# Optimization experiments

Hardware: AMD Instinct MI355X
Metric: run time of the kernel (lower is better)

## Reference

```python
import jax, jax.numpy as jnp
import numpy as np

B, T, HID, MC, L, NCLS = 256, 128, 64, 30, 2, 100


def _flow(x, t, fW0, fb0, fW1, fb1, fW2, fb2, ftw):
    # Continuous affine coupling flow (stribor). x: [..., S, HID], t: [..., S, 1]
    hid = x.shape[-1]
    base = (jnp.arange(hid) < hid // 2).astype(x.dtype)  # ordered_0 mask
    for l in range(fW0.shape[0]):
        m = base if l % 2 == 0 else 1.0 - base
        z = x * m
        a = jnp.tanh(jnp.concatenate([z, t], -1) @ fW0[l] + fb0[l])
        a = jnp.tanh(a @ fW1[l] + fb1[l])
        ss = a @ fW2[l] + fb2[l]                      # [..., 2*hid]
        scale, shift = jnp.split(ss, 2, -1)
        t_scale, t_shift = jnp.split(jnp.tanh(t * ftw[l]), 2, -1)  # TimeTanh
        x = z + (1.0 - m) * (x * jnp.exp(scale * t_scale) + shift * t_shift)
    return x


def setup_inputs() -> dict:
    key = jax.random.key(0)
    ks = jax.random.split(key, 12)
    n = lambda k, s, sc=0.1: jax.random.normal(k, s, dtype=jnp.float32) * sc
    return {
        "times": jax.random.uniform(ks[0], (B, T, 1), dtype=jnp.float32),
        "marks": jax.random.randint(ks[1], (B, T, 1), 0, NCLS),
        "mask": jnp.ones((B, T, 1), jnp.float32),
        "u": jax.random.uniform(ks[2], (T, MC, 1), dtype=jnp.float32),
        "emb": n(ks[3], (NCLS, HID), 1.0),
        "fW0": n(ks[4], (L, HID + 1, HID)),
        "fb0": jnp.zeros((L, HID), jnp.float32),
        "fW1": n(ks[5], (L, HID, HID)),
        "fb1": jnp.zeros((L, HID), jnp.float32),
        "fW2": n(ks[6], (L, HID, 2 * HID)),
        "fb2": jnp.zeros((L, 2 * HID), jnp.float32),
        "ftw": n(ks[7], (L, 2 * HID), 1.0),
        "Wi": n(ks[8], (HID, 1)),
        "bi": jnp.zeros((1,), jnp.float32),
        "W_ih": n(ks[9], (4 * HID, 1 + HID)),
        "W_hh": n(ks[10], (4 * HID, HID)),
        "b_ih": jnp.zeros((4 * HID,), jnp.float32),
        "b_hh": jnp.zeros((4 * HID,), jnp.float32),
    }


def reference(times, marks, mask, u, emb, fW0, fb0, fW1, fb1, fW2, fb2, ftw,
              Wi, bi, W_ih, W_hh, b_ih, b_hh):
    Bn, Tn, _ = times.shape
    hid = emb.shape[1]
    mc = u.shape[1]
    marks_e = emb[marks[..., 0]]      # [B,T,hid]
    m1 = marks_e[:, 1]                # source uses marks[:, 1] every step (faithful)
    inten = lambda x: jax.nn.softplus(x @ Wi + bi)

    def step(carry, xs):
        h, c = carry                  # h,c: [B,hid]
        t, u_i = xs                   # t: [B,1], u_i: [mc,1]
        t3 = t[:, None, :]            # [B,1,1]
        ts = u_i[None] * t3           # [B,mc,1] MC time samples in [0,t)
        xb = jnp.broadcast_to(h[:, None, :], (Bn, mc, hid))
        path = _flow(xb, ts, fW0, fb0, fW1, fb1, fW2, fb2, ftw)   # [B,mc,hid]
        integral = inten(path).mean(1, keepdims=True) * t3        # [B,1,1]
        h2 = _flow(h[:, None, :], t3, fW0, fb0, fW1, fb1, fW2, fb2, ftw)  # [B,1,hid]
        lam = inten(h2)                                           # [B,1,1]
        gates = jnp.concatenate([t, m1], -1) @ W_ih.T + b_ih + h2[:, 0] @ W_hh.T + b_hh
        ig, fg, gg, og = jnp.split(gates, 4, -1)
        c_n = jax.nn.sigmoid(fg) * c + jax.nn.sigmoid(ig) * jnp.tanh(gg)
        h_n = jax.nn.sigmoid(og) * jnp.tanh(c_n)
        nll = -jnp.log(lam[:, 0]) + integral[:, 0]                # [B,1]
        return (h_n, c_n), (h2[:, 0], nll)

    h0 = jnp.zeros((Bn, hid), times.dtype)
    (_, _), (hidden, nll) = jax.lax.scan(step, (h0, h0), (jnp.swapaxes(times, 0, 1), u))
    hidden = jnp.swapaxes(hidden, 0, 1)                           # [B,T,hid]
    loss = (jnp.swapaxes(nll, 0, 1)[:, :, :] * mask[..., 0][..., None]).sum() / mask.sum()
    return loss, hidden
```

## Files before the change

### kernel.cpp

```cpp
#include <hip/hip_runtime.h>
#include <hip/hip_bf16.h>
#include <math.h>

#define Bn   256
#define Tn   128
#define HID  64
#define MCn  30

typedef __attribute__((ext_vector_type(8))) short bf16x8;
typedef __attribute__((ext_vector_type(4))) float f32x4;

__device__ __forceinline__ float rcp_(float x) { return __builtin_amdgcn_rcpf(x); }
__device__ __forceinline__ float tanhf_(float x) {
    float e = __expf(-2.0f * x);
    return __builtin_fmaf(2.0f, rcp_(1.0f + e), -1.0f);
}
__device__ __forceinline__ float sigmoidf_(float x) {
    return rcp_(1.0f + __expf(-x));
}
__device__ __forceinline__ float softplusf_(float z) {
    float e = __expf(-fabsf(z));
    return fmaxf(z, 0.0f) + __logf(1.0f + e);
}
__device__ __forceinline__ unsigned short f2b(float f) {
    union { float f; unsigned u; } v; v.f = f;
    unsigned r = v.u + 0x7FFF + ((v.u >> 16) & 1);
    return (unsigned short)(r >> 16);
}
__device__ __forceinline__ unsigned pk2(float a, float b) {
    union { __hip_bfloat162 h2; unsigned u; } cv;
    cv.h2 = __float22bfloat162_rn(make_float2(a, b));
    return cv.u;
}

extern "C" __global__ __launch_bounds__(256)
void prep_kernel(const int* __restrict__ marks, const float* __restrict__ mask,
                 const float* __restrict__ emb, const float* __restrict__ fW0,
                 const float* __restrict__ fW1, const float* __restrict__ fW2,
                 const float* __restrict__ fb0, const float* __restrict__ fb1,
                 const float* __restrict__ fb2, const float* __restrict__ ftw,
                 const float* __restrict__ Wi, const float* __restrict__ W_ih,
                 const float* __restrict__ W_hh,
                 const float* __restrict__ b_ih, const float* __restrict__ b_hh,
                 float* __restrict__ gc, float* __restrict__ invd,
                 float* __restrict__ parv, unsigned short* __restrict__ parwb,
                 float* __restrict__ seqw1T, float* __restrict__ seqw2T,
                 float* __restrict__ whh260)
{
    __shared__ float red[4];
    const int blk = blockIdx.x, tid = threadIdx.x;
    if (blk < Bn) {
        const int mark = marks[blk * Tn + 1];
        const float* er = emb + mark * HID;
        const float* wr = W_ih + tid * 65 + 1;
        float acc = b_ih[tid] + b_hh[tid];
        #pragma unroll
        for (int k = 0; k < HID; k++) acc += er[k] * wr[k];
        gc[blk * 256 + tid] = acc;
    } else if (blk == Bn) {
        float s = 0.f;
        for (int i = tid; i < Bn * Tn; i += 256) s += mask[i];
        #pragma unroll
        for (int off = 32; off >= 1; off >>= 1) s += __shfl_xor(s, off, 64);
        if ((tid & 63) == 0) red[tid >> 6] = s;
        __syncthreads();
        if (tid == 0) invd[0] = 1.0f / (red[0] + red[1] + red[2] + red[3]);
    } else if (blk == Bn + 1) {
        if (tid < 128) {
            int l = tid >> 6, m = tid & 63;
            parv[tid]       = fb0[tid];
            parv[128 + tid] = fW0[(l * 65 + 64) * 64 + m];
            parv[256 + tid] = fb1[tid];
            int act = 32 * (1 - l);
            parv[384 + tid] = fb2[l * 128 + act + (m & 31) + 64 * (m >> 5)];
        }
        if (tid < 64) {
            int l = tid >> 5, i2 = tid & 31, act = 32 * (1 - l);
            parv[512 + tid] = ftw[l * 128 + act + i2];
            parv[576 + tid] = ftw[l * 128 + 64 + act + i2];
            parv[640 + tid] = Wi[tid];
            parv[704 + tid] = 0.f;
        }
    } else if (blk == Bn + 2) {
        for (int i = tid; i < 5120; i += 256) {
            int k = i % 40, m = (i / 40) & 63, l = i / 2560;
            float v = (k < 32) ? fW0[(l * 65 + 32 * l + k) * 64 + m] : 0.f;
            parwb[i] = f2b(v);
        }
    } else if (blk == Bn + 3) {
        for (int i = tid; i < 9216; i += 256) {
            int k = i % 72, m = (i / 72) & 63, l = i / 4608;
            float v = (k < 64) ? fW1[(l * 64 + k) * 64 + m] : 0.f;
            parwb[5120 + i] = f2b(v);
        }
    } else if (blk == Bn + 4) {
        for (int i = tid; i < 9216; i += 256) {
            int k = i % 72, m = (i / 72) & 63, l = i / 4608;
            int act = 32 * (1 - l);
            float v = (k < 64) ? fW2[(l * 64 + k) * 128 + act + (m & 31) + 64 * (m >> 5)] : 0.f;
            parwb[14336 + i] = f2b(v);
        }
    } else if (blk == Bn + 5) {
        for (int i = tid; i < 8704; i += 256) {
            int k = i % 68, j = (i / 68) & 63, l = i / 4352;
            seqw1T[i] = (k < 64) ? fW1[(l * 64 + k) * 64 + j] : 0.f;
        }
    } else if (blk == Bn + 6) {
        for (int i = tid; i < 8704; i += 256) {
            int k = i % 68, j = (i / 68) & 63, l = i / 4352;
            int act = 32 * (1 - l);
            seqw2T[i] = (k < 64) ?
                fW2[(l * 64 + k) * 128 + act + (j & 31) + 64 * (j >> 5)] : 0.f;
        }
    } else {
        for (int i = tid; i < 16640; i += 256) {
            int j = i / 260, rem = i % 260, k = rem >> 2, r = rem & 3;
            whh260[i] = (k < 64) ? W_hh[(r * 64 + j) * 64 + k] : 0.f;
        }
    }
}

extern "C" __global__ __launch_bounds__(192, 1)
void fused_kernel(const float* __restrict__ times, const float* __restrict__ mask,
                  const float* __restrict__ u,
                  const float* __restrict__ fW0, const float* __restrict__ fb0,
                  const float* __restrict__ fb1, const float* __restrict__ fb2,
                  const float* __restrict__ ftw, const float* __restrict__ Wi,
                  const float* __restrict__ bi, const float* __restrict__ W_ih,
                  const float* __restrict__ gc, const float* __restrict__ seqw1T,
                  const float* __restrict__ parv,
                  const unsigned short* __restrict__ parwb,
                  const float* __restrict__ invd, float* __restrict__ out)
{
    const int tid  = threadIdx.x;
    const int lane = tid & 63;
    const int w    = tid >> 6;
    const int b    = blockIdx.x;
    const int quad = lane >> 4, l15 = lane & 15;

    extern __shared__ float smem[];
    float* w1l  = smem;
    float* w2l  = smem + 8704;
    float* whhl = smem + 17408;
    float* tl   = smem + 34048;
    float* ml   = smem + 34176;
    float* xl   = smem + 34304;
    float* al   = smem + 34368;
    float* ssl  = smem + 34432;
    float* hbuf = smem + 34496;
    float* pr   = smem + 34624;
    unsigned short* csact = (unsigned short*)(smem + 34628);
    unsigned short* csxk1 = csact + 2304;
    unsigned short* csx0  = csxk1 + 1280;

    {
        const float4* s = (const float4*)seqw1T;
        float4* d = (float4*)smem;
        for (int i = tid; i < 8512; i += 192) d[i] = s[i];
        for (int i = tid; i < 128; i += 192) {
            tl[i] = times[b * Tn + i];
            ml[i] = mask[b * Tn + i];
        }
    }

    const float bi0 = bi[0];
    const float idn = invd[0];

    float w0c[2][32], w0tc[2], b0c[2], b1c[2], b2c[2], ftsc[2], ftsh[2];
    float wih0[4], gcr[4], wij = 0.f;
    float h = 0.f, c = 0.f, nllacc = 0.f;
    if (w == 0) {
        #pragma unroll
        for (int l = 0; l < 2; l++) {
            #pragma unroll
            for (int kk = 0; kk < 32; kk++)
                w0c[l][kk] = fW0[(l * 65 + 32 * l + kk) * 64 + lane];
            w0tc[l] = fW0[(l * 65 + 64) * 64 + lane];
            b0c[l]  = fb0[l * 64 + lane];
            b1c[l]  = fb1[l * 64 + lane];
            const int act = 32 * (1 - l);
            b2c[l]  = fb2[l * 128 + act + (lane & 31) + 64 * (lane >> 5)];
            ftsc[l] = ftw[l * 128 + lane];
            ftsh[l] = ftw[l * 128 + 64 + lane];
        }
        wij = Wi[lane];
        #pragma unroll
        for (int r = 0; r < 4; r++) {
            wih0[r] = W_ih[(r * 64 + lane) * 65];
            gcr[r]  = gc[b * 256 + r * 64 + lane];
        }
    }
    const int cw = w - 1;
    unsigned short* myact = csact + cw * 1152;
    unsigned short* myxk  = csxk1 + cw * 640;
    unsigned short* myx0  = csx0  + cw * 40;
    const int mc  = cw * 16 + l15;
    const bool valmc = (w > 0) && (mc < MCn);
    float wacc = 0.f;

    __syncthreads();

    for (int t = 0; t < Tn; t++) {
        if (w == 0) hbuf[(t & 1) * 64 + lane] = h;
        __syncthreads();

        if (w == 0) {
            const float tb = tl[t];
            float tscv[2], tshv[2];
            #pragma unroll
            for (int l = 0; l < 2; l++) {
                tscv[l] = tanhf_(tb * ftsc[l]);
                tshv[l] = tanhf_(tb * ftsh[l]);
            }
            float x = h;
            xl[lane] = x;
            #pragma unroll
            for (int l = 0; l < 2; l++) {
                const int kb  = 32 * l;
                const int act = 32 * (1 - l);
                {
                    float p0 = b0c[l] + tb * w0tc[l], p1 = 0.f, p2 = 0.f, p3 = 0.f;
                    const float4* xv4 = (const float4*)(xl + kb);
                    #pragma unroll
                    for (int k4 = 0; k4 < 8; k4++) {
                        float4 xv = xv4[k4];
                        p0 += xv.x * w0c[l][4 * k4 + 0];
                        p1 += xv.y * w0c[l][4 * k4 + 1];
                        p2 += xv.z * w0c[l][4 * k4 + 2];
                        p3 += xv.w * w0c[l][4 * k4 + 3];
                    }
                    al[lane] = tanhf_((p0 + p1) + (p2 + p3));
                }
                {
                    float p0 = b1c[l], p1 = 0.f, p2 = 0.f, p3 = 0.f;
                    const float4* av4 = (const float4*)al;
                    const float*  wp  = w1l + (l * 64 + lane) * 68;
                    #pragma unroll
                    for (int k4 = 0; k4 < 16; k4++) {
                        float4 av = av4[k4];
                        float4 wv = *(const float4*)(wp + 4 * k4);
                        p0 += av.x * wv.x; p1 += av.y * wv.y;
                        p2 += av.z * wv.z; p3 += av.w * wv.w;
                    }
                    al[lane] = tanhf_((p0 + p1) + (p2 + p3));
                }
                {
                    float p0 = b2c[l], p1 = 0.f, p2 = 0.f, p3 = 0.f;
                    const float4* av4 = (const float4*)al;
                    const float*  wp  = w2l + (l * 64 + lane) * 68;
                    #pragma unroll
                    for (int k4 = 0; k4 < 16; k4++) {
                        float4 av = av4[k4];
                        float4 wv = *(const float4*)(wp + 4 * k4);
                        p0 += av.x * wv.x; p1 += av.y * wv.y;
                        p2 += av.z * wv.z; p3 += av.w * wv.w;
                    }
                    ssl[lane] = (p0 + p1) + (p2 + p3);
                }
                const int idx = (lane - act) & 31;
                const float scl = ssl[idx];
                const float shf = ssl[idx + 32];
                const float xa  = x * __expf(scl * tscv[l]) + shf * tshv[l];
                const bool active = (l == 0) ? (lane >= 32) : (lane < 32);
                x = active ? xa : x;
                xl[lane] = x;
            }
            out[1 + (b * Tn + t) * 64 + lane] = x;
            float v = x * wij;
            #pragma unroll
            for (int off = 32; off >= 1; off >>= 1) v += __shfl_xor(v, off, 64);
            nllacc += -__logf(softplusf_(v + bi0)) * ml[t];
            float g0 = gcr[0] + tb * wih0[0];
            float g1 = gcr[1] + tb * wih0[1];
            float g2 = gcr[2] + tb * wih0[2];
            float g3 = gcr[3] + tb * wih0[3];
            {
                const float*  wr_base = whhl + lane * 260;
                const float4* hv4 = (const float4*)xl;
                #pragma unroll
                for (int k4 = 0; k4 < 16; k4++) {
                    float4 hv = hv4[k4];
                    const float* wr = wr_base + 16 * k4;
                    float4 wa = *(const float4*)(wr);
                    float4 wb = *(const float4*)(wr + 4);
                    float4 wc = *(const float4*)(wr + 8);
                    float4 wd = *(const float4*)(wr + 12);
                    g0 += hv.x * wa.x; g1 += hv.x * wa.y; g2 += hv.x * wa.z; g3 += hv.x * wa.w;
                    g0 += hv.y * wb.x; g1 += hv.y * wb.y; g2 += hv.y * wb.z; g3 += hv.y * wb.w;
                    g0 += hv.z * wc.x; g1 += hv.z * wc.y; g2 += hv.z * wc.z; g3 += hv.z * wc.w;
                    g0 += hv.w * wd.x; g1 += hv.w * wd.y; g2 += hv.w * wd.z; g3 += hv.w * wd.w;
                }
            }
            c = sigmoidf_(g1) * c + sigmoidf_(g0) * tanhf_(g2);
            h = sigmoidf_(g3) * tanhf_(c);
        } else {
            const float tb = tl[t];
            const float ts   = valmc ? u[t * MCn + mc] * tb : 0.f;
            const float sclf = valmc ? tb * (1.0f / 30.0f) * idn * ml[t] : 0.f;
            const float* hb  = hbuf + (t & 1) * 64;
            f32x4 xr[4];
            #pragma unroll
            for (int mt = 0; mt < 4; mt++)
                xr[mt] = *(const f32x4*)(hb + mt * 16 + quad * 4);
            if (lane < 32) myx0[lane] = f2b(hb[lane]);
            #pragma unroll
            for (int l = 0; l < 2; l++) {
                const unsigned short* wA1 = parwb + l * 2560;
                const unsigned short* wA2 = parwb + 5120 + l * 4608;
                const unsigned short* wA3 = parwb + 14336 + l * 4608;
                f32x4 c1[4];
                {
                    bf16x8 bfin = (l == 0) ? *(const bf16x8*)(myx0 + quad * 8)
                                           : *(const bf16x8*)(myxk + l15 * 40 + quad * 8);
                    #pragma unroll
                    for (int mt = 0; mt < 4; mt++) {
                        bf16x8 af = *(const bf16x8*)(wA1 + (mt * 16 + l15) * 40 + quad * 8);
                        f32x4 z = {0.f, 0.f, 0.f, 0.f};
                        c1[mt] = __builtin_amdgcn_mfma_f32_16x16x32_bf16(af, bfin, z, 0, 0, 0);
                    }
                }
                #pragma unroll
                for (int mt = 0; mt < 4; mt++) {
                    f32x4 b0r = *(const f32x4*)(parv + 0   + l * 64 + mt * 16 + quad * 4);
                    f32x4 w0r = *(const f32x4*)(parv + 128 + l * 64 + mt * 16 + quad * 4);
                    float v0 = tanhf_(c1[mt][0] + b0r[0] + ts * w0r[0]);
                    float v1 = tanhf_(c1[mt][1] + b0r[1] + ts * w0r[1]);
                    float v2 = tanhf_(c1[mt][2] + b0r[2] + ts * w0r[2]);
                    float v3 = tanhf_(c1[mt][3] + b0r[3] + ts * w0r[3]);
                    uint2 pk; pk.x = pk2(v0, v1); pk.y = pk2(v2, v3);
                    *(uint2*)(myact + l15 * 72 + mt * 16 + quad * 4) = pk;
                }
                f32x4 cc[4];
                #pragma unroll
                for (int mt = 0; mt < 4; mt++) cc[mt] = (f32x4){0.f, 0.f, 0.f, 0.f};
                #pragma unroll
                for (int kt = 0; kt < 2; kt++) {
                    bf16x8 bfa = *(const bf16x8*)(myact + l15 * 72 + kt * 32 + quad * 8);
                    #pragma unroll
                    for (int mt = 0; mt < 4; mt++) {
                        bf16x8 af = *(const bf16x8*)(wA2 + (mt * 16 + l15) * 72 + kt * 32 + quad * 8);
                        cc[mt] = __builtin_amdgcn_mfma_f32_16x16x32_bf16(af, bfa, cc[mt], 0, 0, 0);
                    }
                }
                #pragma unroll
                for (int mt = 0; mt < 4; mt++) {
                    f32x4 b1r = *(const f32x4*)(parv + 256 + l * 64 + mt * 16 + quad * 4);
                    float v0 = tanhf_(cc[mt][0] + b1r[0]);
                    float v1 = tanhf_(cc[mt][1] + b1r[1]);
                    float v2 = tanhf_(cc[mt][2] + b1r[2]);
                    float v3 = tanhf_(cc[mt][3] + b1r[3]);
                    uint2 pk; pk.x = pk2(v0, v1); pk.y = pk2(v2, v3);
                    *(uint2*)(myact + l15 * 72 + mt * 16 + quad * 4) = pk;
                }
                f32x4 ssf[4];
                #pragma unroll
                for (int mt = 0; mt < 4; mt++) ssf[mt] = (f32x4){0.f, 0.f, 0.f, 0.f};
                #pragma unroll
                for (int kt = 0; kt < 2; kt++) {
                    bf16x8 bfa = *(const bf16x8*)(myact + l15 * 72 + kt * 32 + quad * 8);
                    #pragma unroll
                    for (int mt = 0; mt < 4; mt++) {
                        bf16x8 af = *(const bf16x8*)(wA3 + (mt * 16 + l15) * 72 + kt * 32 + quad * 8);
                        ssf[mt] = __builtin_amdgcn_mfma_f32_16x16x32_bf16(af, bfa, ssf[mt], 0, 0, 0);
                    }
                }
                #pragma unroll
                for (int mt2 = 0; mt2 < 2; mt2++) {
                    f32x4 b2s = *(const f32x4*)(parv + 384 + l * 64 +      mt2 * 16 + quad * 4);
                    f32x4 b2h = *(const f32x4*)(parv + 384 + l * 64 + 32 + mt2 * 16 + quad * 4);
                    f32x4 fa  = *(const f32x4*)(parv + 512 + l * 32 + mt2 * 16 + quad * 4);
                    f32x4 fb  = *(const f32x4*)(parv + 576 + l * 32 + mt2 * 16 + quad * 4);
                    const int xm = (l == 0) ? (mt2 + 2) : mt2;
                    #pragma unroll
                    for (int r = 0; r < 4; r++) {
                        float sc  = ssf[mt2][r] + b2s[r];
                        float sh  = ssf[mt2 + 2][r] + b2h[r];
                        float tsc = tanhf_(ts * fa[r]);
                        float tsh = tanhf_(ts * fb[r]);
                        xr[xm][r] = xr[xm][r] * __expf(sc * tsc) + sh * tsh;
                    }
                    if (l == 0) {
                        uint2 pk;
                        pk.x = pk2(xr[xm][0], xr[xm][1]);
                        pk.y = pk2(xr[xm][2], xr[xm][3]);
                        *(uint2*)(myxk + l15 * 40 + mt2 * 16 + quad * 4) = pk;
                    }
                }
            }
            float d0 = 0.f, d1 = 0.f;
            #pragma unroll
            for (int mt = 0; mt < 4; mt++) {
                f32x4 wi4 = *(const f32x4*)(parv + 640 + mt * 16 + quad * 4);
                d0 += xr[mt][0] * wi4[0] + xr[mt][2] * wi4[2];
                d1 += xr[mt][1] * wi4[1] + xr[mt][3] * wi4[3];
            }
            float d = d0 + d1;
            d += __shfl_xor(d, 16, 64);
            d += __shfl_xor(d, 32, 64);
            if (quad == 0) wacc += softplusf_(d + bi0) * sclf;
        }
    }
    if (w == 0) {
        if (lane == 0) pr[0] = nllacc * idn;
    } else {
        #pragma unroll
        for (int off = 1; off <= 32; off <<= 1) wacc += __shfl_xor(wacc, off, 64);
        if (lane == 0) pr[w] = wacc;
    }
    __syncthreads();
    if (tid == 0) atomicAdd(out, pr[0] + pr[1] + pr[2]);
}

extern "C" void kernel_launch(void* const* d_in, const int* in_sizes, int n_in,
                              void* d_out, int out_size, void* d_ws, size_t ws_size,
                              hipStream_t stream)
{
    const float* times = (const float*)d_in[0];
    const int*   marks = (const int*)  d_in[1];
    const float* mask  = (const float*)d_in[2];
    const float* u     = (const float*)d_in[3];
    const float* emb   = (const float*)d_in[4];
    const float* fW0   = (const float*)d_in[5];
    const float* fb0   = (const float*)d_in[6];
    const float* fW1   = (const float*)d_in[7];
    const float* fb1   = (const float*)d_in[8];
    const float* fW2   = (const float*)d_in[9];
    const float* fb2   = (const float*)d_in[10];
    const float* ftw   = (const float*)d_in[11];
    const float* Wi    = (const float*)d_in[12];
    const float* bi    = (const float*)d_in[13];
    const float* W_ih  = (const float*)d_in[14];
    const float* W_hh  = (const float*)d_in[15];
    const float* b_ih  = (const float*)d_in[16];
    const float* b_hh  = (const float*)d_in[17];
    float* out = (float*)d_out;

    float* wsp     = (float*)d_ws;
    float* gc      = wsp;
    float* invd    = gc + 65536;
    float* seqw1T  = invd + 4;
    float* seqw2T  = seqw1T + 8704;
    float* whh260  = seqw2T + 8704;
    float* parv    = whh260 + 16640;
    unsigned short* parwb = (unsigned short*)(parv + 768);

    hipMemsetAsync(d_out, 0, sizeof(float), stream);

    const int FUSED_SMEM = 34628 * 4 + 7328;
    hipFuncSetAttribute((const void*)fused_kernel,
                        hipFuncAttributeMaxDynamicSharedMemorySize, FUSED_SMEM);

    prep_kernel<<<Bn + 8, 256, 0, stream>>>(marks, mask, emb, fW0, fW1, fW2,
                                            fb0, fb1, fb2, ftw, Wi, W_ih, W_hh,
                                            b_ih, b_hh, gc, invd, parv, parwb,
                                            seqw1T, seqw2T, whh260);
    fused_kernel<<<Bn, 192, FUSED_SMEM, stream>>>(times, mask, u, fW0, fb0,
                                                  fb1, fb2, ftw, Wi, bi, W_ih,
                                                  gc, seqw1T, parv, parwb,
                                                  invd, out);
}
```

Before: 616.7 us.

## Pipeline sequential LSTM producer ahead of MC flow consumers in chunks

The per-step block barrier between the serial recurrence wave and the two Monte Carlo flow waves is replaced by a chunked producer/consumer schedule. Wave 0 computes the hidden states for the next 8 steps into a double-buffered shared buffer while the consumer waves process the current chunk. Consumers now handle two time steps per iteration, which doubles the MFMA N-dimension work per weight fetch. Barriers drop from one per step to one per chunk, at the cost of more shared memory and register pressure and a pipeline fill for the first chunk.

```diff
diff --git a/kernel.cpp b/kernel.cpp
--- a/kernel.cpp
+++ b/kernel.cpp
@@ -6,6 +6,8 @@
 #define Tn   128
 #define HID  64
 #define MCn  30
+#define CH   8
+#define NCH  (Tn / CH)
 
 typedef __attribute__((ext_vector_type(8))) short bf16x8;
 typedef __attribute__((ext_vector_type(4))) float f32x4;
@@ -148,10 +150,8 @@
     float* al   = smem + 34368;
     float* ssl  = smem + 34432;
     float* hbuf = smem + 34496;
-    float* pr   = smem + 34624;
-    unsigned short* csact = (unsigned short*)(smem + 34628);
-    unsigned short* csxk1 = csact + 2304;
-    unsigned short* csx0  = csxk1 + 1280;
+    float* pr   = smem + 35520;
+    unsigned short* cbase = (unsigned short*)(smem + 35524);
 
     {
         const float4* s = (const float4*)seqw1T;
@@ -168,7 +168,7 @@
 
     float w0c[2][32], w0tc[2], b0c[2], b1c[2], b2c[2], ftsc[2], ftsh[2];
     float wih0[4], gcr[4], wij = 0.f;
-    float h = 0.f, c = 0.f, nllacc = 0.f;
+    float h = 0.f, c_ = 0.f, nllacc = 0.f;
     if (w == 0) {
         #pragma unroll
         for (int l = 0; l < 2; l++) {
@@ -191,20 +191,19 @@
         }
     }
     const int cw = w - 1;
-    unsigned short* myact = csact + cw * 1152;
-    unsigned short* myxk  = csxk1 + cw * 640;
-    unsigned short* myx0  = csx0  + cw * 40;
-    const int mc  = cw * 16 + l15;
+    unsigned short* myact = cbase + cw * 3664;
+    unsigned short* myxk  = myact + 2304;
+    unsigned short* myx0  = myxk + 1280;
+    const int mc = cw * 16 + l15;
     const bool valmc = (w > 0) && (mc < MCn);
     float wacc = 0.f;
 
-    __syncthreads();
-
-    for (int t = 0; t < Tn; t++) {
-        if (w == 0) hbuf[(t & 1) * 64 + lane] = h;
-        __syncthreads();
-
-        if (w == 0) {
+    auto produce_chunk = [&](int c) {
+        float* hbw = hbuf + (c & 1) * (CH * 64);
+        #pragma unroll 1
+        for (int s = 0; s < CH; s++) {
+            const int t = c * CH + s;
+            hbw[s * 64 + lane] = h;
             const float tb = tl[t];
             float tscv[2], tshv[2];
             #pragma unroll
@@ -291,77 +290,123 @@
                     g0 += hv.w * wd.x; g1 += hv.w * wd.y; g2 += hv.w * wd.z; g3 += hv.w * wd.w;
                 }
             }
-            c = sigmoidf_(g1) * c + sigmoidf_(g0) * tanhf_(g2);
-            h = sigmoidf_(g3) * tanhf_(c);
-        } else {
-            const float tb = tl[t];
-            const float ts   = valmc ? u[t * MCn + mc] * tb : 0.f;
-            const float sclf = valmc ? tb * (1.0f / 30.0f) * idn * ml[t] : 0.f;
-            const float* hb  = hbuf + (t & 1) * 64;
-            f32x4 xr[4];
-            #pragma unroll
-            for (int mt = 0; mt < 4; mt++)
-                xr[mt] = *(const f32x4*)(hb + mt * 16 + quad * 4);
-            if (lane < 32) myx0[lane] = f2b(hb[lane]);
+            c_ = sigmoidf_(g1) * c_ + sigmoidf_(g0) * tanhf_(g2);
+            h  = sigmoidf_(g3) * tanhf_(c_);
+        }
+    };
+
+    auto consume_chunk = [&](int c) {
+        const float* hbc = hbuf + (c & 1) * (CH * 64);
+        #pragma unroll 1
+        for (int i = 0; i < CH / 2; i++) {
+            const int t0 = c * CH + 2 * i;
+            float tbv[2], tsv[2], sclf[2];
+            const float* hb[2];
+            #pragma unroll
+            for (int nt = 0; nt < 2; nt++) {
+                const int tt = t0 + nt;
+                tbv[nt] = tl[tt];
+                tsv[nt]  = valmc ? u[tt * MCn + mc] * tbv[nt] : 0.f;
+                sclf[nt] = valmc ? tbv[nt] * (1.0f / 30.0f) * idn * ml[tt] : 0.f;
+                hb[nt] = hbc + (2 * i + nt) * 64;
+            }
+            {
+                const int nt = lane >> 5, li = lane & 31;
+                myx0[nt * 40 + li] = f2b(hb[nt][li]);
+            }
+            f32x4 xr[2][4];
+            #pragma unroll
+            for (int nt = 0; nt < 2; nt++)
+                #pragma unroll
+                for (int mt = 0; mt < 4; mt++)
+                    xr[nt][mt] = *(const f32x4*)(hb[nt] + mt * 16 + quad * 4);
+
             #pragma unroll
             for (int l = 0; l < 2; l++) {
                 const unsigned short* wA1 = parwb + l * 2560;
                 const unsigned short* wA2 = parwb + 5120 + l * 4608;
                 const unsigned short* wA3 = parwb + 14336 + l * 4608;
-                f32x4 c1[4];
+                f32x4 c1[4][2];
                 {
-                    bf16x8 bfin = (l == 0) ? *(const bf16x8*)(myx0 + quad * 8)
-                                           : *(const bf16x8*)(myxk + l15 * 40 + quad * 8);
+                    bf16x8 bf[2];
+                    #pragma unroll
+                    for (int nt = 0; nt < 2; nt++)
+                        bf[nt] = (l == 0)
+                            ? *(const bf16x8*)(myx0 + nt * 40 + quad * 8)
+                            : *(const bf16x8*)(myxk + (nt * 16 + l15) * 40 + quad * 8);
                     #pragma unroll
                     for (int mt = 0; mt < 4; mt++) {
                         bf16x8 af = *(const bf16x8*)(wA1 + (mt * 16 + l15) * 40 + quad * 8);
-                        f32x4 z = {0.f, 0.f, 0.f, 0.f};
-                        c1[mt] = __builtin_amdgcn_mfma_f32_16x16x32_bf16(af, bfin, z, 0, 0, 0);
+                        #pragma unroll
+                        for (int nt = 0; nt < 2; nt++) {
+                            f32x4 z = {0.f, 0.f, 0.f, 0.f};
+                            c1[mt][nt] = __builtin_amdgcn_mfma_f32_16x16x32_bf16(af, bf[nt], z, 0, 0, 0);
+                        }
                     }
                 }
                 #pragma unroll
                 for (int mt = 0; mt < 4; mt++) {
                     f32x4 b0r = *(const f32x4*)(parv + 0   + l * 64 + mt * 16 + quad * 4);
                     f32x4 w0r = *(const f32x4*)(parv + 128 + l * 64 + mt * 16 + quad * 4);
-                    float v0 = tanhf_(c1[mt][0] + b0r[0] + ts * w0r[0]);
-                    float v1 = tanhf_(c1[mt][1] + b0r[1] + ts * w0r[1]);
-                    float v2 = tanhf_(c1[mt][2] + b0r[2] + ts * w0r[2]);
-                    float v3 = tanhf_(c1[mt][3] + b0r[3] + ts * w0r[3]);
-                    uint2 pk; pk.x = pk2(v0, v1); pk.y = pk2(v2, v3);
-                    *(uint2*)(myact + l15 * 72 + mt * 16 + quad * 4) = pk;
-                }
-                f32x4 cc[4];
-                #pragma unroll
-                for (int mt = 0; mt < 4; mt++) cc[mt] = (f32x4){0.f, 0.f, 0.f, 0.f};
+                    #pragma unroll
+                    for (int nt = 0; nt < 2; nt++) {
+                        float v0 = tanhf_(c1[mt][nt][0] + b0r[0] + tsv[nt] * w0r[0]);
+                        float v1 = tanhf_(c1[mt][nt][1] + b0r[1] + tsv[nt] * w0r[1]);
+                        float v2 = tanhf_(c1[mt][nt][2] + b0r[2] + tsv[nt] * w0r[2]);
+                        float v3 = tanhf_(c1[mt][nt][3] + b0r[3] + tsv[nt] * w0r[3]);
+                        uint2 pk; pk.x = pk2(v0, v1); pk.y = pk2(v2, v3);
+                        *(uint2*)(myact + (nt * 16 + l15) * 72 + mt * 16 + quad * 4) = pk;
+                    }
+                }
+                f32x4 cc[4][2];
+                #pragma unroll
+                for (int mt = 0; mt < 4; mt++)
+                    #pragma unroll
+                    for (int nt = 0; nt < 2; nt++) cc[mt][nt] = (f32x4){0.f, 0.f, 0.f, 0.f};
                 #pragma unroll
                 for (int kt = 0; kt < 2; kt++) {
-                    bf16x8 bfa = *(const bf16x8*)(myact + l15 * 72 + kt * 32 + quad * 8);
+                    bf16x8 bf[2];
+                    #pragma unroll
+                    for (int nt = 0; nt < 2; nt++)
+                        bf[nt] = *(const bf16x8*)(myact + (nt * 16 + l15) * 72 + kt * 32 + quad * 8);
                     #pragma unroll
                     for (int mt = 0; mt < 4; mt++) {
                         bf16x8 af = *(const bf16x8*)(wA2 + (mt * 16 + l15) * 72 + kt * 32 + quad * 8);
-                        cc[mt] = __builtin_amdgcn_mfma_f32_16x16x32_bf16(af, bfa, cc[mt], 0, 0, 0);
+                        #pragma unroll
+                        for (int nt = 0; nt < 2; nt++)
+                            cc[mt][nt] = __builtin_amdgcn_mfma_f32_16x16x32_bf16(af, bf[nt], cc[mt][nt], 0, 0, 0);
                     }
                 }
                 #pragma unroll
                 for (int mt = 0; mt < 4; mt++) {
                     f32x4 b1r = *(const f32x4*)(parv + 256 + l * 64 + mt * 16 + quad * 4);
-                    float v0 = tanhf_(cc[mt][0] + b1r[0]);
-                    float v1 = tanhf_(cc[mt][1] + b1r[1]);
-                    float v2 = tanhf_(cc[mt][2] + b1r[2]);
-                    float v3 = tanhf_(cc[mt][3] + b1r[3]);
-                    uint2 pk; pk.x = pk2(v0, v1); pk.y = pk2(v2, v3);
-                    *(uint2*)(myact + l15 * 72 + mt * 16 + quad * 4) = pk;
-                }
-                f32x4 ssf[4];
-                #pragma unroll
-                for (int mt = 0; mt < 4; mt++) ssf[mt] = (f32x4){0.f, 0.f, 0.f, 0.f};
+                    #pragma unroll
+                    for (int nt = 0; nt < 2; nt++) {
+                        float v0 = tanhf_(cc[mt][nt][0] + b1r[0]);
+                        float v1 = tanhf_(cc[mt][nt][1] + b1r[1]);
+                        float v2 = tanhf_(cc[mt][nt][2] + b1r[2]);
+                        float v3 = tanhf_(cc[mt][nt][3] + b1r[3]);
+                        uint2 pk; pk.x = pk2(v0, v1); pk.y = pk2(v2, v3);
+                        *(uint2*)(myact + (nt * 16 + l15) * 72 + mt * 16 + quad * 4) = pk;
+                    }
+                }
+                f32x4 ssf[4][2];
+                #pragma unroll
+                for (int mt = 0; mt < 4; mt++)
+                    #pragma unroll
+                    for (int nt = 0; nt < 2; nt++) ssf[mt][nt] = (f32x4){0.f, 0.f, 0.f, 0.f};
                 #pragma unroll
                 for (int kt = 0; kt < 2; kt++) {
-                    bf16x8 bfa = *(const bf16x8*)(myact + l15 * 72 + kt * 32 + quad * 8);
+                    bf16x8 bf[2];
+                    #pragma unroll
+                    for (int nt = 0; nt < 2; nt++)
+                        bf[nt] = *(const bf16x8*)(myact + (nt * 16 + l15) * 72 + kt * 32 + quad * 8);
                     #pragma unroll
                     for (int mt = 0; mt < 4; mt++) {
                         bf16x8 af = *(const bf16x8*)(wA3 + (mt * 16 + l15) * 72 + kt * 32 + quad * 8);
-                        ssf[mt] = __builtin_amdgcn_mfma_f32_16x16x32_bf16(af, bfa, ssf[mt], 0, 0, 0);
+                        #pragma unroll
+                        for (int nt = 0; nt < 2; nt++)
+                            ssf[mt][nt] = __builtin_amdgcn_mfma_f32_16x16x32_bf16(af, bf[nt], ssf[mt][nt], 0, 0, 0);
                     }
                 }
                 #pragma unroll
@@ -372,34 +417,53 @@
                     f32x4 fb  = *(const f32x4*)(parv + 576 + l * 32 + mt2 * 16 + quad * 4);
                     const int xm = (l == 0) ? (mt2 + 2) : mt2;
                     #pragma unroll
-                    for (int r = 0; r < 4; r++) {
-                        float sc  = ssf[mt2][r] + b2s[r];
-                        float sh  = ssf[mt2 + 2][r] + b2h[r];
-                        float tsc = tanhf_(ts * fa[r]);
-                        float tsh = tanhf_(ts * fb[r]);
-                        xr[xm][r] = xr[xm][r] * __expf(sc * tsc) + sh * tsh;
-                    }
-                    if (l == 0) {
-                        uint2 pk;
-                        pk.x = pk2(xr[xm][0], xr[xm][1]);
-                        pk.y = pk2(xr[xm][2], xr[xm][3]);
-                        *(uint2*)(myxk + l15 * 40 + mt2 * 16 + quad * 4) = pk;
-                    }
-                }
-            }
-            float d0 = 0.f, d1 = 0.f;
-            #pragma unroll
-            for (int mt = 0; mt < 4; mt++) {
-                f32x4 wi4 = *(const f32x4*)(parv + 640 + mt * 16 + quad * 4);
-                d0 += xr[mt][0] * wi4[0] + xr[mt][2] * wi4[2];
-                d1 += xr[mt][1] * wi4[1] + xr[mt][3] * wi4[3];
-            }
-            float d = d0 + d1;
-            d += __shfl_xor(d, 16, 64);
-            d += __shfl_xor(d, 32, 64);
-            if (quad == 0) wacc += softplusf_(d + bi0) * sclf;
-        }
+                    for (int nt = 0; nt < 2; nt++) {
+                        #pragma unroll
+                        for (int r = 0; r < 4; r++) {
+                            float sc  = ssf[mt2][nt][r] + b2s[r];
+                            float sh  = ssf[mt2 + 2][nt][r] + b2h[r];
+                            float tsc = tanhf_(tsv[nt] * fa[r]);
+                            float tsh = tanhf_(tsv[nt] * fb[r]);
+                            xr[nt][xm][r] = xr[nt][xm][r] * __expf(sc * tsc) + sh * tsh;
+                        }
+                        if (l == 0) {
+                            uint2 pk;
+                            pk.x = pk2(xr[nt][xm][0], xr[nt][xm][1]);
+                            pk.y = pk2(xr[nt][xm][2], xr[nt][xm][3]);
+                            *(uint2*)(myxk + (nt * 16 + l15) * 40 + mt2 * 16 + quad * 4) = pk;
+                        }
+                    }
+                }
+            }
+            #pragma unroll
+            for (int nt = 0; nt < 2; nt++) {
+                float d0 = 0.f, d1 = 0.f;
+                #pragma unroll
+                for (int mt = 0; mt < 4; mt++) {
+                    f32x4 wi4 = *(const f32x4*)(parv + 640 + mt * 16 + quad * 4);
+                    d0 += xr[nt][mt][0] * wi4[0] + xr[nt][mt][2] * wi4[2];
+                    d1 += xr[nt][mt][1] * wi4[1] + xr[nt][mt][3] * wi4[3];
+                }
+                float d = d0 + d1;
+                d += __shfl_xor(d, 16, 64);
+                d += __shfl_xor(d, 32, 64);
+                if (quad == 0) wacc += softplusf_(d + bi0) * sclf[nt];
+            }
+        }
+    };
+
+    __syncthreads();
+    if (w == 0) produce_chunk(0);
+    __syncthreads();
+    for (int c = 0; c < NCH; c++) {
+        if (w == 0) {
+            if (c + 1 < NCH) produce_chunk(c + 1);
+        } else {
+            consume_chunk(c);
+        }
+        __syncthreads();
     }
+
     if (w == 0) {
         if (lane == 0) pr[0] = nllacc * idn;
     } else {
@@ -446,7 +510,7 @@
 
     hipMemsetAsync(d_out, 0, sizeof(float), stream);
 
-    const int FUSED_SMEM = 34628 * 4 + 7328;
+    const int FUSED_SMEM = 35524 * 4 + 7328 * 2;
     hipFuncSetAttribute((const void*)fused_kernel,
                         hipFuncAttributeMaxDynamicSharedMemorySize, FUSED_SMEM);
 
```

Result: faster. 600.6 us (-2.6%).

## Pipeline recurrent wave and MC waves in chunks of eight steps

Applied to the files above, without the earlier changes.

The serial LSTM/flow recurrence on wave 0 now produces hidden states for a chunk of eight timesteps into a double-buffered shared buffer, while the two Monte Carlo waves consume the previous chunk. Block-wide barriers drop from one per timestep to one per chunk. The aim is to cut synchronisation overhead and let the recurrence overlap with the integral computation. It adds a one-chunk prologue that is not overlapped, and it changes the shared-memory layout.

```diff
diff --git a/kernel.cpp b/kernel.cpp
--- a/kernel.cpp
+++ b/kernel.cpp
@@ -6,6 +6,8 @@
 #define Tn   128
 #define HID  64
 #define MCn  30
+#define CH   8
+#define NCH  (Tn / CH)
 
 typedef __attribute__((ext_vector_type(8))) short bf16x8;
 typedef __attribute__((ext_vector_type(4))) float f32x4;
@@ -148,10 +150,8 @@
     float* al   = smem + 34368;
     float* ssl  = smem + 34432;
     float* hbuf = smem + 34496;
-    float* pr   = smem + 34624;
-    unsigned short* csact = (unsigned short*)(smem + 34628);
-    unsigned short* csxk1 = csact + 2304;
-    unsigned short* csx0  = csxk1 + 1280;
+    float* pr   = smem + 35520;
+    unsigned short* cbase = (unsigned short*)(smem + 35524);
 
     {
         const float4* s = (const float4*)seqw1T;
@@ -168,7 +168,7 @@
 
     float w0c[2][32], w0tc[2], b0c[2], b1c[2], b2c[2], ftsc[2], ftsh[2];
     float wih0[4], gcr[4], wij = 0.f;
-    float h = 0.f, c = 0.f, nllacc = 0.f;
+    float h = 0.f, c_ = 0.f, nllacc = 0.f;
     if (w == 0) {
         #pragma unroll
         for (int l = 0; l < 2; l++) {
@@ -191,20 +191,19 @@
         }
     }
     const int cw = w - 1;
-    unsigned short* myact = csact + cw * 1152;
-    unsigned short* myxk  = csxk1 + cw * 640;
-    unsigned short* myx0  = csx0  + cw * 40;
-    const int mc  = cw * 16 + l15;
+    unsigned short* myact = cbase + cw * 1832;
+    unsigned short* myxk  = myact + 1152;
+    unsigned short* myx0  = myxk + 640;
+    const int mc = cw * 16 + l15;
     const bool valmc = (w > 0) && (mc < MCn);
     float wacc = 0.f;
 
-    __syncthreads();
-
-    for (int t = 0; t < Tn; t++) {
-        if (w == 0) hbuf[(t & 1) * 64 + lane] = h;
-        __syncthreads();
-
-        if (w == 0) {
+    auto produce_chunk = [&](int c) {
+        float* hbw = hbuf + (c & 1) * (CH * 64);
+        #pragma unroll 1
+        for (int s = 0; s < CH; s++) {
+            const int t = c * CH + s;
+            hbw[s * 64 + lane] = h;
             const float tb = tl[t];
             float tscv[2], tshv[2];
             #pragma unroll
@@ -291,13 +290,20 @@
                     g0 += hv.w * wd.x; g1 += hv.w * wd.y; g2 += hv.w * wd.z; g3 += hv.w * wd.w;
                 }
             }
-            c = sigmoidf_(g1) * c + sigmoidf_(g0) * tanhf_(g2);
-            h = sigmoidf_(g3) * tanhf_(c);
-        } else {
+            c_ = sigmoidf_(g1) * c_ + sigmoidf_(g0) * tanhf_(g2);
+            h  = sigmoidf_(g3) * tanhf_(c_);
+        }
+    };
+
+    auto consume_chunk = [&](int c) {
+        const float* hbc = hbuf + (c & 1) * (CH * 64);
+        #pragma unroll 1
+        for (int s = 0; s < CH; s++) {
+            const int t = c * CH + s;
             const float tb = tl[t];
             const float ts   = valmc ? u[t * MCn + mc] * tb : 0.f;
             const float sclf = valmc ? tb * (1.0f / 30.0f) * idn * ml[t] : 0.f;
-            const float* hb  = hbuf + (t & 1) * 64;
+            const float* hb  = hbc + s * 64;
             f32x4 xr[4];
             #pragma unroll
             for (int mt = 0; mt < 4; mt++)
@@ -399,7 +405,20 @@
             d += __shfl_xor(d, 32, 64);
             if (quad == 0) wacc += softplusf_(d + bi0) * sclf;
         }
+    };
+
+    __syncthreads();
+    if (w == 0) produce_chunk(0);
+    __syncthreads();
+    for (int c = 0; c < NCH; c++) {
+        if (w == 0) {
+            if (c + 1 < NCH) produce_chunk(c + 1);
+        } else {
+            consume_chunk(c);
+        }
+        __syncthreads();
     }
+
     if (w == 0) {
         if (lane == 0) pr[0] = nllacc * idn;
     } else {
@@ -446,7 +465,7 @@
 
     hipMemsetAsync(d_out, 0, sizeof(float), stream);
 
-    const int FUSED_SMEM = 34628 * 4 + 7328;
+    const int FUSED_SMEM = 35524 * 4 + 1832 * 2 * 2;
     hipFuncSetAttribute((const void*)fused_kernel,
                         hipFuncAttributeMaxDynamicSharedMemorySize, FUSED_SMEM);
 
```

New measurement: 625.0 us. No clear change (+1.4%).

## Replace per-step block barrier with LDS flag handshake between LSTM and MC waves

Applied to the files above, without the earlier changes.

Removes the __syncthreads at every timestep and splits the loop so wave 0 (sequential flow+LSTM) and waves 1-2 (Monte Carlo integral) run independent loops. They coordinate through shared-memory progress counters with sleep-spin waits. hbuf is double-buffered, so wave 0 can run up to one step ahead of the MC waves instead of waiting in lockstep. Per-wave scratch buffers are regrouped contiguously. This risks memory-ordering issues, since volatile LDS flags with only a block fence may not order LDS writes correctly, and it adds spin overhead.

```diff
diff --git a/kernel.cpp b/kernel.cpp
--- a/kernel.cpp
+++ b/kernel.cpp
@@ -149,9 +149,8 @@
     float* ssl  = smem + 34432;
     float* hbuf = smem + 34496;
     float* pr   = smem + 34624;
-    unsigned short* csact = (unsigned short*)(smem + 34628);
-    unsigned short* csxk1 = csact + 2304;
-    unsigned short* csx0  = csxk1 + 1280;
+    volatile unsigned* flg = (volatile unsigned*)(smem + 34628);
+    unsigned short* cbase = (unsigned short*)(smem + 34632);
 
     {
         const float4* s = (const float4*)seqw1T;
@@ -161,6 +160,7 @@
             tl[i] = times[b * Tn + i];
             ml[i] = mask[b * Tn + i];
         }
+        if (tid < 3) flg[tid] = 0;
     }
 
     const float bi0 = bi[0];
@@ -168,7 +168,7 @@
 
     float w0c[2][32], w0tc[2], b0c[2], b1c[2], b2c[2], ftsc[2], ftsh[2];
     float wih0[4], gcr[4], wij = 0.f;
-    float h = 0.f, c = 0.f, nllacc = 0.f;
+    float h = 0.f, c_ = 0.f, nllacc = 0.f;
     if (w == 0) {
         #pragma unroll
         for (int l = 0; l < 2; l++) {
@@ -191,20 +191,24 @@
         }
     }
     const int cw = w - 1;
-    unsigned short* myact = csact + cw * 1152;
-    unsigned short* myxk  = csxk1 + cw * 640;
-    unsigned short* myx0  = csx0  + cw * 40;
+    unsigned short* myact = cbase + cw * 1832;
+    unsigned short* myxk  = myact + 1152;
+    unsigned short* myx0  = myxk + 640;
     const int mc  = cw * 16 + l15;
     const bool valmc = (w > 0) && (mc < MCn);
     float wacc = 0.f;
 
     __syncthreads();
 
-    for (int t = 0; t < Tn; t++) {
-        if (w == 0) hbuf[(t & 1) * 64 + lane] = h;
-        __syncthreads();
-
-        if (w == 0) {
+    if (w == 0) {
+        for (int t = 0; t < Tn; t++) {
+            if (t >= 2) {
+                const unsigned need = (unsigned)(t - 1);
+                while (flg[1] < need || flg[2] < need) __builtin_amdgcn_s_sleep(1);
+                __threadfence_block();
+            }
+            hbuf[(t & 1) * 64 + lane] = h;
+            if (lane == 0) flg[0] = (unsigned)(t + 1);
             const float tb = tl[t];
             float tscv[2], tshv[2];
             #pragma unroll
@@ -291,9 +295,13 @@
                     g0 += hv.w * wd.x; g1 += hv.w * wd.y; g2 += hv.w * wd.z; g3 += hv.w * wd.w;
                 }
             }
-            c = sigmoidf_(g1) * c + sigmoidf_(g0) * tanhf_(g2);
-            h = sigmoidf_(g3) * tanhf_(c);
-        } else {
+            c_ = sigmoidf_(g1) * c_ + sigmoidf_(g0) * tanhf_(g2);
+            h  = sigmoidf_(g3) * tanhf_(c_);
+        }
+    } else {
+        for (int t = 0; t < Tn; t++) {
+            while (flg[0] < (unsigned)(t + 1)) __builtin_amdgcn_s_sleep(1);
+            __threadfence_block();
             const float tb = tl[t];
             const float ts   = valmc ? u[t * MCn + mc] * tb : 0.f;
             const float sclf = valmc ? tb * (1.0f / 30.0f) * idn * ml[t] : 0.f;
@@ -398,8 +406,10 @@
             d += __shfl_xor(d, 16, 64);
             d += __shfl_xor(d, 32, 64);
             if (quad == 0) wacc += softplusf_(d + bi0) * sclf;
+            if (lane == 0) flg[w] = (unsigned)(t + 1);
         }
     }
+
     if (w == 0) {
         if (lane == 0) pr[0] = nllacc * idn;
     } else {
@@ -446,7 +456,7 @@
 
     hipMemsetAsync(d_out, 0, sizeof(float), stream);
 
-    const int FUSED_SMEM = 34628 * 4 + 7328;
+    const int FUSED_SMEM = 34632 * 4 + 7328;
     hipFuncSetAttribute((const void*)fused_kernel,
                         hipFuncAttributeMaxDynamicSharedMemorySize, FUSED_SMEM);
 
```

After: 582.6 us, median of 2. 5.5% less time.
